# Optimization experiments

Measured on AMD Instinct MI355X. Metric: run time of the kernel, lower is better.

## Reference

```python
import jax, jax.numpy as jnp
import numpy as np

G = 8192   # number of groups / clusters of samples
S = 64     # samples per group
N = G * S
D = 128
H = 256
K = 8      # n_clusters
EPS = 0.01


def setup_inputs() -> dict:
    key = jax.random.key(0)
    ks = jax.random.split(key, 6)
    index = jnp.repeat(jnp.arange(G, dtype=jnp.int32), S)  # sorted, contiguous groups
    x = jax.random.normal(ks[0], (N, D), dtype=jnp.float32)
    y = jax.random.normal(ks[1], (N, 1), dtype=jnp.float32)
    anchor_x = jax.random.normal(ks[2], (G, D), dtype=jnp.float32)
    anchor_y = jax.random.normal(ks[3], (G, 1), dtype=jnp.float32)
    W1 = jax.random.normal(ks[4], (D, H), dtype=jnp.float32) / np.sqrt(D)
    b1 = jnp.zeros((H,), jnp.float32)
    W2 = jax.random.normal(ks[5], (H, K + 2), dtype=jnp.float32) / np.sqrt(H)
    b2 = jnp.zeros((K + 2,), jnp.float32)
    return {"index": index, "x": x, "y": y, "anchor_x": anchor_x,
            "anchor_y": anchor_y, "W1": W1, "b1": b1, "W2": W2, "b2": b2}


def reference(index, x, y, anchor_x, anchor_y, W1, b1, W2, b2):
    idx = index
    # repeat_interleave(anchor, sizes) == gather for sorted contiguous index
    x_rel = x - anchor_x[idx]            # [N, D]
    y_rel = y - anchor_y[idx]            # [N, 1]

    seg = lambda v: jax.ops.segment_sum(v, idx, num_segments=G)
    n = seg(jnp.ones((x.shape[0], 1), x.dtype))          # [G, 1] group sizes
    sx = seg(x_rel)                                       # [G, D]
    sy = seg(y_rel)                                       # [G, 1]
    sxy = seg(x_rel * y_rel)                              # [G, D]
    # per-group unbiased cross-covariance cov(x, y)
    cov = (sxy - sx * sy / n) / (n - 1.0)                 # [G, D]

    # per-group scalar variance of x_rel flattened over [n_g, D] (torch .var())
    sxx = seg((x_rel * x_rel).sum(-1, keepdims=True))     # [G, 1]
    tot = sx.sum(-1, keepdims=True)                       # [G, 1]
    nD = n * x.shape[1]
    var = (sxx - tot * tot / nD) / (nD - 1.0)             # [G, 1]

    rep = cov / var                                       # xtxinv * representation

    # MLP head (Tanh hidden, dropout is identity at inference)
    h = jnp.tanh(rep @ W1 + b1)
    out = h @ W2 + b2                                     # [G, K+2]
    alpha = jax.nn.softplus(out[:, :1]) * (1.0 - EPS) + EPS
    beta = jax.nn.softplus(out[:, 1:2]) * (1.0 - EPS) + EPS
    mixture = jax.nn.softmax(out[:, 2:], axis=-1)         # [G, K]
    scale = jnp.sqrt(beta / alpha)                        # sqrt(1/precision_mean)
    # Gamma(alpha, beta) / Categorical(mixture) returned via their parameters
    return (rep, mixture, scale, alpha, beta)
```

## Files before the change

### kernel.cpp

```cpp
#include <hip/hip_runtime.h>
#include <math.h>

#define NG   8192
#define NS   64
#define ND   128
#define NH   256
#define NO   10
#define GPB  16
#define WPB  4

typedef float floatx4 __attribute__((ext_vector_type(4)));

__global__ __launch_bounds__(256) void stats_kernel(
    const float* __restrict__ x, const float* __restrict__ y,
    const float* __restrict__ ax, const float* __restrict__ ay,
    float* __restrict__ rep)
{
    const int t    = threadIdx.x;
    const int w    = t >> 6;
    const int l    = t & 63;
    const int g    = blockIdx.x * WPB + w;
    const int c    = l & 31;
    const int half = l >> 5;

    __shared__ float yrelL[WPB][NS];

    float yv = y[g * NS + l] - ay[g];
    yrelL[w][l] = yv;

    const floatx4 a4 = ((const floatx4*)ax)[g * 32 + c];
    const floatx4* xg = (const floatx4*)x
                      + (size_t)g * (NS * 32) + (size_t)(half * 32) * 32 + c;

    floatx4 S   = (floatx4)(0.f);
    floatx4 Sxy = (floatx4)(0.f);
    float   S2  = 0.f;

#pragma unroll
    for (int ii = 0; ii < 4; ++ii) {
        floatx4 xv[8];
#pragma unroll
        for (int j = 0; j < 8; ++j)
            xv[j] = __builtin_nontemporal_load(&xg[(ii * 8 + j) * 32]);
#pragma unroll
        for (int j = 0; j < 8; ++j) {
            const float yr = yrelL[w][half * 32 + ii * 8 + j];
            S   += xv[j];
            Sxy += xv[j] * yr;
            S2  += xv[j].x * xv[j].x + xv[j].y * xv[j].y
                 + xv[j].z * xv[j].z + xv[j].w * xv[j].w;
        }
    }

    float sxxc = S2 - 2.0f * (a4.x * S.x + a4.y * S.y + a4.z * S.z + a4.w * S.w)
               + 32.0f * (a4.x * a4.x + a4.y * a4.y + a4.z * a4.z + a4.w * a4.w);
    float totc = (S.x + S.y + S.z + S.w) - 32.0f * (a4.x + a4.y + a4.z + a4.w);

#pragma unroll
    for (int off = 32; off >= 1; off >>= 1) {
        totc += __shfl_xor(totc, off);
        sxxc += __shfl_xor(sxxc, off);
        yv   += __shfl_xor(yv,   off);
    }

    S.x   += __shfl_xor(S.x,   32); S.y   += __shfl_xor(S.y,   32);
    S.z   += __shfl_xor(S.z,   32); S.w   += __shfl_xor(S.w,   32);
    Sxy.x += __shfl_xor(Sxy.x, 32); Sxy.y += __shfl_xor(Sxy.y, 32);
    Sxy.z += __shfl_xor(Sxy.z, 32); Sxy.w += __shfl_xor(Sxy.w, 32);

    const float var = (sxxc - totc * totc * (1.0f / 8192.0f)) * (1.0f / 8191.0f);
    const float iv  = 1.0f / var;
    const float c0  = yv * (1.0f / 64.0f);
    floatx4 rp;
    rp.x = (Sxy.x - S.x * c0) * (1.0f / 63.0f) * iv;
    rp.y = (Sxy.y - S.y * c0) * (1.0f / 63.0f) * iv;
    rp.z = (Sxy.z - S.z * c0) * (1.0f / 63.0f) * iv;
    rp.w = (Sxy.w - S.w * c0) * (1.0f / 63.0f) * iv;
    if (half == 0) ((floatx4*)rep)[g * 32 + c] = rp;
}

__device__ __forceinline__ float fast_tanh(float v) {
    v = fminf(15.0f, fmaxf(-15.0f, v));
    float e = __expf(2.0f * v);
    return (e - 1.0f) / (e + 1.0f);
}

__device__ __forceinline__ float softplus_f(float v) {
    if (v > 15.0f) return v;
    return log1pf(__expf(v));
}

__global__ __launch_bounds__(256) void mlp_kernel(
    const float* __restrict__ rep, const float* __restrict__ W1,
    const float* __restrict__ b1, const float* __restrict__ W2,
    const float* __restrict__ b2, float* __restrict__ mix,
    float* __restrict__ scl, float* __restrict__ alp,
    float* __restrict__ bet)
{
    const int g0 = blockIdx.x * GPB;
    const int t = threadIdx.x;

    __shared__ __align__(16) float repL[GPB][ND];
    __shared__ float hL[GPB][NH + 1];
    __shared__ float w2L[NH * NO];
    __shared__ float outL[GPB][NO];

    {
        const float4* rp4 = (const float4*)(rep + (size_t)g0 * ND);
        float4* dst = (float4*)&repL[0][0];
        dst[t] = rp4[t];
        dst[t + 256] = rp4[t + 256];
    }
    for (int i = t; i < NH * NO; i += 256) w2L[i] = W2[i];
    __syncthreads();

    float acc[GPB];
#pragma unroll
    for (int g = 0; g < GPB; ++g) acc[g] = 0.f;

    for (int d = 0; d < ND; d += 4) {
        float w0 = W1[(d + 0) * NH + t];
        float w1 = W1[(d + 1) * NH + t];
        float w2 = W1[(d + 2) * NH + t];
        float w3 = W1[(d + 3) * NH + t];
#pragma unroll
        for (int g = 0; g < GPB; ++g) {
            const float4 r4 = *(const float4*)&repL[g][d];
            acc[g] += r4.x * w0 + r4.y * w1 + r4.z * w2 + r4.w * w3;
        }
    }
    const float bb = b1[t];
#pragma unroll
    for (int g = 0; g < GPB; ++g) {
        hL[g][t] = fast_tanh(acc[g] + bb);
    }
    __syncthreads();

    if (t < GPB * NO) {
        const int g = t / NO;
        const int k = t - g * NO;
        float s = b2[k];
#pragma unroll 8
        for (int j = 0; j < NH; ++j) s += hL[g][j] * w2L[j * NO + k];
        outL[g][k] = s;
    }
    __syncthreads();

    if (t < GPB) {
        const int gg = g0 + t;
        float al = softplus_f(outL[t][0]) * 0.99f + 0.01f;
        float be = softplus_f(outL[t][1]) * 0.99f + 0.01f;
        float m = -1e30f;
#pragma unroll
        for (int k = 0; k < 8; ++k) m = fmaxf(m, outL[t][2 + k]);
        float e[8];
        float sum = 0.f;
#pragma unroll
        for (int k = 0; k < 8; ++k) { e[k] = __expf(outL[t][2 + k] - m); sum += e[k]; }
        float inv = 1.0f / sum;
#pragma unroll
        for (int k = 0; k < 8; ++k) mix[gg * 8 + k] = e[k] * inv;
        alp[gg] = al;
        bet[gg] = be;
        scl[gg] = sqrtf(be / al);
    }
}

extern "C" void kernel_launch(void* const* d_in, const int* in_sizes, int n_in,
                              void* d_out, int out_size, void* d_ws, size_t ws_size,
                              hipStream_t stream) {
    const float* x  = (const float*)d_in[1];
    const float* y  = (const float*)d_in[2];
    const float* ax = (const float*)d_in[3];
    const float* ay = (const float*)d_in[4];
    const float* W1 = (const float*)d_in[5];
    const float* b1 = (const float*)d_in[6];
    const float* W2 = (const float*)d_in[7];
    const float* b2 = (const float*)d_in[8];

    float* out = (float*)d_out;
    float* rep = out;
    float* mix = out + (size_t)NG * ND;
    float* scl = mix + (size_t)NG * 8;
    float* alp = scl + NG;
    float* bet = alp + NG;

    stats_kernel<<<NG / WPB, 256, 0, stream>>>(x, y, ax, ay, rep);
    mlp_kernel<<<NG / GPB, 256, 0, stream>>>(rep, W1, b1, W2, b2, mix, scl, alp, bet);
}
```

Measured before the change: 381.5 us.

## Fuse per-group statistics and MLP head into a single kernel

Merges the stats kernel and the MLP kernel into one launch. Each block keeps its 4 groups' rep vectors in shared memory and runs the MLP head on them directly, with the second layer reduced by wave shuffles. This removes a kernel launch and the write-then-reread of rep between kernels. In exchange, W1 (128 KB) is now read by every one of the 2048 blocks instead of 512, each block amortises the weight reads over only 4 groups rather than 16, and the larger shared-memory footprint may reduce occupancy during the bandwidth-bound stats phase.

Measured after the change: 380.0 us. No clear change (-0.4%).

```diff
diff --git a/kernel.cpp b/kernel.cpp
--- a/kernel.cpp
+++ b/kernel.cpp
@@ -6,15 +6,29 @@
 #define ND   128
 #define NH   256
 #define NO   10
-#define GPB  16
 #define WPB  4
 
 typedef float floatx4 __attribute__((ext_vector_type(4)));
 
-__global__ __launch_bounds__(256) void stats_kernel(
+__device__ __forceinline__ float fast_tanh(float v) {
+    v = fminf(15.0f, fmaxf(-15.0f, v));
+    float e = __expf(2.0f * v);
+    return (e - 1.0f) / (e + 1.0f);
+}
+
+__device__ __forceinline__ float softplus_f(float v) {
+    if (v > 15.0f) return v;
+    return log1pf(__expf(v));
+}
+
+__global__ __launch_bounds__(256) void fused_kernel(
     const float* __restrict__ x, const float* __restrict__ y,
     const float* __restrict__ ax, const float* __restrict__ ay,
-    float* __restrict__ rep)
+    const float* __restrict__ W1, const float* __restrict__ b1,
+    const float* __restrict__ W2, const float* __restrict__ b2,
+    float* __restrict__ rep, float* __restrict__ mix,
+    float* __restrict__ scl, float* __restrict__ alp,
+    float* __restrict__ bet)
 {
     const int t    = threadIdx.x;
     const int w    = t >> 6;
@@ -24,6 +38,8 @@
     const int half = l >> 5;
 
     __shared__ float yrelL[WPB][NS];
+    __shared__ __align__(16) float repL[WPB][ND];
+    __shared__ float hL[WPB][NH];
 
     float yv = y[g * NS + l] - ay[g];
     yrelL[w][l] = yv;
@@ -76,93 +92,77 @@
     rp.y = (Sxy.y - S.y * c0) * (1.0f / 63.0f) * iv;
     rp.z = (Sxy.z - S.z * c0) * (1.0f / 63.0f) * iv;
     rp.w = (Sxy.w - S.w * c0) * (1.0f / 63.0f) * iv;
-    if (half == 0) ((floatx4*)rep)[g * 32 + c] = rp;
-}
-
-__device__ __forceinline__ float fast_tanh(float v) {
-    v = fminf(15.0f, fmaxf(-15.0f, v));
-    float e = __expf(2.0f * v);
-    return (e - 1.0f) / (e + 1.0f);
-}
-
-__device__ __forceinline__ float softplus_f(float v) {
-    if (v > 15.0f) return v;
-    return log1pf(__expf(v));
-}
-
-__global__ __launch_bounds__(256) void mlp_kernel(
-    const float* __restrict__ rep, const float* __restrict__ W1,
-    const float* __restrict__ b1, const float* __restrict__ W2,
-    const float* __restrict__ b2, float* __restrict__ mix,
-    float* __restrict__ scl, float* __restrict__ alp,
-    float* __restrict__ bet)
-{
-    const int g0 = blockIdx.x * GPB;
-    const int t = threadIdx.x;
-
-    __shared__ __align__(16) float repL[GPB][ND];
-    __shared__ float hL[GPB][NH + 1];
-    __shared__ float w2L[NH * NO];
-    __shared__ float outL[GPB][NO];
-
-    {
-        const float4* rp4 = (const float4*)(rep + (size_t)g0 * ND);
-        float4* dst = (float4*)&repL[0][0];
-        dst[t] = rp4[t];
-        dst[t + 256] = rp4[t + 256];
-    }
-    for (int i = t; i < NH * NO; i += 256) w2L[i] = W2[i];
-    __syncthreads();
-
-    float acc[GPB];
-#pragma unroll
-    for (int g = 0; g < GPB; ++g) acc[g] = 0.f;
-
-    for (int d = 0; d < ND; d += 4) {
-        float w0 = W1[(d + 0) * NH + t];
-        float w1 = W1[(d + 1) * NH + t];
-        float w2 = W1[(d + 2) * NH + t];
-        float w3 = W1[(d + 3) * NH + t];
-#pragma unroll
-        for (int g = 0; g < GPB; ++g) {
-            const float4 r4 = *(const float4*)&repL[g][d];
-            acc[g] += r4.x * w0 + r4.y * w1 + r4.z * w2 + r4.w * w3;
-        }
-    }
-    const float bb = b1[t];
-#pragma unroll
-    for (int g = 0; g < GPB; ++g) {
-        hL[g][t] = fast_tanh(acc[g] + bb);
+    if (half == 0) {
+        ((floatx4*)rep)[g * 32 + c] = rp;
+        ((floatx4*)&repL[w][0])[c]  = rp;
     }
     __syncthreads();
 
-    if (t < GPB * NO) {
-        const int g = t / NO;
-        const int k = t - g * NO;
-        float s = b2[k];
+    {
+        const int j = (w << 6) + l;
+        float acc0 = 0.f, acc1 = 0.f, acc2 = 0.f, acc3 = 0.f;
+        const floatx4* rl0 = (const floatx4*)&repL[0][0];
+        const floatx4* rl1 = (const floatx4*)&repL[1][0];
+        const floatx4* rl2 = (const floatx4*)&repL[2][0];
+        const floatx4* rl3 = (const floatx4*)&repL[3][0];
 #pragma unroll 8
-        for (int j = 0; j < NH; ++j) s += hL[g][j] * w2L[j * NO + k];
-        outL[g][k] = s;
+        for (int d4 = 0; d4 < 32; ++d4) {
+            const float w0  = W1[(4 * d4 + 0) * NH + j];
+            const float w1v = W1[(4 * d4 + 1) * NH + j];
+            const float w2v = W1[(4 * d4 + 2) * NH + j];
+            const float w3v = W1[(4 * d4 + 3) * NH + j];
+            floatx4 r;
+            r = rl0[d4]; acc0 += r.x * w0 + r.y * w1v + r.z * w2v + r.w * w3v;
+            r = rl1[d4]; acc1 += r.x * w0 + r.y * w1v + r.z * w2v + r.w * w3v;
+            r = rl2[d4]; acc2 += r.x * w0 + r.y * w1v + r.z * w2v + r.w * w3v;
+            r = rl3[d4]; acc3 += r.x * w0 + r.y * w1v + r.z * w2v + r.w * w3v;
+        }
+        const float bb = b1[j];
+        hL[0][j] = fast_tanh(acc0 + bb);
+        hL[1][j] = fast_tanh(acc1 + bb);
+        hL[2][j] = fast_tanh(acc2 + bb);
+        hL[3][j] = fast_tanh(acc3 + bb);
     }
     __syncthreads();
 
-    if (t < GPB) {
-        const int gg = g0 + t;
-        float al = softplus_f(outL[t][0]) * 0.99f + 0.01f;
-        float be = softplus_f(outL[t][1]) * 0.99f + 0.01f;
-        float m = -1e30f;
+    {
+        float s[NO];
 #pragma unroll
-        for (int k = 0; k < 8; ++k) m = fmaxf(m, outL[t][2 + k]);
-        float e[8];
-        float sum = 0.f;
+        for (int k = 0; k < NO; ++k) s[k] = 0.f;
 #pragma unroll
-        for (int k = 0; k < 8; ++k) { e[k] = __expf(outL[t][2 + k] - m); sum += e[k]; }
-        float inv = 1.0f / sum;
+        for (int u = 0; u < 4; ++u) {
+            const int j = l + (u << 6);
+            const float hv = hL[w][j];
+            const float* w2row = &W2[j * NO];
 #pragma unroll
-        for (int k = 0; k < 8; ++k) mix[gg * 8 + k] = e[k] * inv;
-        alp[gg] = al;
-        bet[gg] = be;
-        scl[gg] = sqrtf(be / al);
+            for (int k = 0; k < NO; ++k) s[k] += hv * w2row[k];
+        }
+#pragma unroll
+        for (int k = 0; k < NO; ++k) {
+#pragma unroll
+            for (int off = 32; off >= 1; off >>= 1)
+                s[k] += __shfl_xor(s[k], off);
+        }
+        if (l == 0) {
+            float o[NO];
+#pragma unroll
+            for (int k = 0; k < NO; ++k) o[k] = s[k] + b2[k];
+            const float al = softplus_f(o[0]) * 0.99f + 0.01f;
+            const float be = softplus_f(o[1]) * 0.99f + 0.01f;
+            float m = -1e30f;
+#pragma unroll
+            for (int k = 0; k < 8; ++k) m = fmaxf(m, o[2 + k]);
+            float e[8];
+            float sum = 0.f;
+#pragma unroll
+            for (int k = 0; k < 8; ++k) { e[k] = __expf(o[2 + k] - m); sum += e[k]; }
+            const float inv = 1.0f / sum;
+#pragma unroll
+            for (int k = 0; k < 8; ++k) mix[g * 8 + k] = e[k] * inv;
+            alp[g] = al;
+            bet[g] = be;
+            scl[g] = sqrtf(be / al);
+        }
     }
 }
 
@@ -185,6 +185,6 @@
     float* alp = scl + NG;
     float* bet = alp + NG;
 
-    stats_kernel<<<NG / WPB, 256, 0, stream>>>(x, y, ax, ay, rep);
-    mlp_kernel<<<NG / GPB, 256, 0, stream>>>(rep, W1, b1, W2, b2, mix, scl, alp, bet);
+    fused_kernel<<<NG / WPB, 256, 0, stream>>>(x, y, ax, ay, W1, b1, W2, b2,
+                                               rep, mix, scl, alp, bet);
 }
```
